# Performance work log

Measured on AMD Instinct MI355X. Metric: run time of the kernel, lower is better.

The kernel has to match this reference:

```python
import jax, jax.numpy as jnp
import numpy as np

B, IN_BITS, NUM_LUTS, K = 1024, 4096, 16384, 6

def setup_inputs() -> dict:
    key = jax.random.key(0)
    k1, k2, k3 = jax.random.split(key, 3)
    x_bits = jax.random.uniform(k1, (B, IN_BITS), dtype=jnp.float32)
    table = jax.random.normal(k2, (NUM_LUTS, 2 ** K), dtype=jnp.float32) * 0.01
    conn_idx = jax.random.randint(k3, (NUM_LUTS, K), 0, IN_BITS, dtype=jnp.int64)
    return {"x_bits": x_bits, "table": table, "conn_idx": conn_idx}

def reference(x_bits, table, conn_idx):
    # threshold to binary bits: [B, IN_BITS]
    bits01 = (x_bits > 0.5)
    # gather connected bits per LUT: [B, NUM_LUTS, K]
    bits = bits01[:, conn_idx]
    # bit-pack (MSB first, matching idx = idx*2 + bit loop): [B, NUM_LUTS]
    powers = (2 ** jnp.arange(K - 1, -1, -1, dtype=jnp.int32))  # [K]
    idx = jnp.sum(bits.astype(jnp.int32) * powers, axis=-1)
    # per-LUT table lookup: table[l, idx[b, l]]
    lut_ids = jnp.arange(NUM_LUTS, dtype=jnp.int32)[None, :]  # [1, NUM_LUTS]
    out = table[lut_ids, idx]  # [B, NUM_LUTS]
    return jax.nn.sigmoid(out)
```

## Files before the change

kernel.cpp:

```cpp
#include <hip/hip_runtime.h>
#include <hip/hip_bf16.h>

constexpr int B        = 1024;
constexpr int IN_BITS  = 4096;
constexpr int NUM_LUTS = 16384;
constexpr int K        = 6;

constexpr int TPB        = 256;
constexpr int LUTS_PER_B = 256;
constexpr int CHUNKS     = 16;
constexpr int BCH        = B / CHUNKS;

constexpr int PACK_BLOCKS = (IN_BITS / TPB) * (B / 32);
constexpr int TBL_BLOCKS  = NUM_LUTS / 64;

__device__ inline unsigned short f2bf(float f) {
    unsigned u = __float_as_uint(f);
    return (unsigned short)((u + 0x7FFFu + ((u >> 16) & 1u)) >> 16);
}

__global__ __launch_bounds__(TPB) void prep_kernel(
    const float* __restrict__ x, const float* __restrict__ table,
    unsigned* __restrict__ packedT, unsigned short* __restrict__ tableT)
{
    __shared__ float tile[64][65];
    const int tid = threadIdx.x;
    const int blk = blockIdx.x;

    if (blk < PACK_BLOCKS) {
        const int pos = (blk % (IN_BITS / TPB)) * TPB + tid;
        const int g   = blk / (IN_BITS / TPB);
        const float* xp = x + (size_t)g * 32 * IN_BITS + pos;
        unsigned word = 0;
#pragma unroll
        for (int j = 0; j < 32; ++j)
            word |= (xp[(size_t)j * IN_BITS] > 0.5f) ? (1u << j) : 0u;
        packedT[(size_t)g * IN_BITS + pos] = word;
    } else {
        const int bt = blk - PACK_BLOCKS;
        const int l0 = bt * 64;
        const float4* src = (const float4*)(table + (size_t)l0 * 64);
#pragma unroll
        for (int i = 0; i < 4; ++i) {
            int q = tid + i * 256;
            float4 v = src[q];
            int l = q >> 4;
            int e = (q & 15) * 4;
            tile[l][e + 0] = v.x; tile[l][e + 1] = v.y;
            tile[l][e + 2] = v.z; tile[l][e + 3] = v.w;
        }
        __syncthreads();
#pragma unroll
        for (int i = 0; i < 4; ++i) {
            int q  = tid + i * 256;
            int e  = q >> 4;
            int lc = (q & 15) * 4;
            ushort4 v;
            v.x = f2bf(1.0f / (1.0f + __expf(-tile[lc + 0][e])));
            v.y = f2bf(1.0f / (1.0f + __expf(-tile[lc + 1][e])));
            v.z = f2bf(1.0f / (1.0f + __expf(-tile[lc + 2][e])));
            v.w = f2bf(1.0f / (1.0f + __expf(-tile[lc + 3][e])));
            ((ushort4*)(tableT + (size_t)e * NUM_LUTS + l0))[q & 15] = v;
        }
    }
}

__global__ __launch_bounds__(TPB, 4) void lut_kernel(
    const int*            __restrict__ conn,
    const unsigned*       __restrict__ packedT,
    const unsigned short* __restrict__ tableT,
    float*                __restrict__ out)
{
    __shared__ unsigned short tbl[64 * LUTS_PER_B];

    const int tid = threadIdx.x;
    const int l0  = blockIdx.x * LUTS_PER_B;
    const int l   = l0 + tid;

    {
        uint4* dst = (uint4*)tbl;
#pragma unroll
        for (int i = 0; i < 8; ++i) {
            int q = tid + i * 256;
            int e = q >> 5;
            int p = q & 31;
            dst[q] = ((const uint4*)(tableT + (size_t)e * NUM_LUTS + l0))[p];
        }
    }

    int c[K];
#pragma unroll
    for (int k = 0; k < K; ++k) c[k] = conn[(size_t)l * K + k];

    __syncthreads();

    const int bbase = blockIdx.y * BCH;
    float* op = out + (size_t)bbase * NUM_LUTS + l;

#pragma unroll
    for (int g = 0; g < BCH / 32; ++g) {
        const unsigned* pr = packedT + (size_t)(bbase / 32 + g) * IN_BITS;
        unsigned w[K];
#pragma unroll
        for (int k = 0; k < K; ++k) w[k] = pr[c[k]];

#pragma unroll
        for (int j = 0; j < 32; ++j) {
            int idx = 0;
#pragma unroll
            for (int k = 0; k < K; ++k)
                idx = (idx << 1) | (int)((w[k] >> j) & 1u);
            unsigned short h = tbl[idx * LUTS_PER_B + tid];
            float v = __uint_as_float((unsigned)h << 16);
            __builtin_nontemporal_store(v, op);
            op += NUM_LUTS;
        }
    }
}

extern "C" void kernel_launch(void* const* d_in, const int* in_sizes, int n_in,
                              void* d_out, int out_size, void* d_ws, size_t ws_size,
                              hipStream_t stream)
{
    const float* x_bits = (const float*)d_in[0];
    const float* table  = (const float*)d_in[1];
    const int*   conn   = (const int*)d_in[2];
    float* out = (float*)d_out;

    unsigned*       packedT = (unsigned*)d_ws;
    unsigned short* tableT  = (unsigned short*)((char*)d_ws + 512 * 1024);

    prep_kernel<<<PACK_BLOCKS + TBL_BLOCKS, TPB, 0, stream>>>(
        x_bits, table, packedT, tableT);

    dim3 g2(NUM_LUTS / LUTS_PER_B, CHUNKS);
    lut_kernel<<<g2, TPB, 0, stream>>>(conn, packedT, tableT, out);
}
```

Before: 93.55 us.

## Fuse prep and LUT kernels into one cooperative kernel with grid sync

Merges the bit-packing/table-transpose prep kernel and the LUT lookup kernel into one cooperatively launched kernel. The grid is 1024 blocks: the first 768 do prep work, then a grid-wide barrier runs before every block does the lookup phase. Both phases share one shared-memory buffer. This removes the second kernel launch and the gap between kernels, but adds a grid barrier and needs all 1024 blocks resident at once. The input x loads also become nontemporal.

```diff
diff --git a/kernel.cpp b/kernel.cpp
--- a/kernel.cpp
+++ b/kernel.cpp
@@ -1,5 +1,8 @@
 #include <hip/hip_runtime.h>
 #include <hip/hip_bf16.h>
+#include <hip/hip_cooperative_groups.h>
+
+namespace cg = cooperative_groups;
 
 constexpr int B        = 1024;
 constexpr int IN_BITS  = 4096;
@@ -13,17 +16,22 @@
 
 constexpr int PACK_BLOCKS = (IN_BITS / TPB) * (B / 32);
 constexpr int TBL_BLOCKS  = NUM_LUTS / 64;
+constexpr int GRID        = (NUM_LUTS / LUTS_PER_B) * CHUNKS;
 
 __device__ inline unsigned short f2bf(float f) {
     unsigned u = __float_as_uint(f);
     return (unsigned short)((u + 0x7FFFu + ((u >> 16) & 1u)) >> 16);
 }
 
-__global__ __launch_bounds__(TPB) void prep_kernel(
-    const float* __restrict__ x, const float* __restrict__ table,
-    unsigned* __restrict__ packedT, unsigned short* __restrict__ tableT)
+__global__ __launch_bounds__(TPB, 4) void fused_kernel(
+    const float*    __restrict__ x,
+    const float*    __restrict__ table,
+    const int*      __restrict__ conn,
+    unsigned*       __restrict__ packedT,
+    unsigned short* __restrict__ tableT,
+    float*          __restrict__ out)
 {
-    __shared__ float tile[64][65];
+    __shared__ char smem[64 * LUTS_PER_B * 2];
     const int tid = threadIdx.x;
     const int blk = blockIdx.x;
 
@@ -33,10 +41,13 @@
         const float* xp = x + (size_t)g * 32 * IN_BITS + pos;
         unsigned word = 0;
 #pragma unroll
-        for (int j = 0; j < 32; ++j)
-            word |= (xp[(size_t)j * IN_BITS] > 0.5f) ? (1u << j) : 0u;
+        for (int j = 0; j < 32; ++j) {
+            float v = __builtin_nontemporal_load(xp + (size_t)j * IN_BITS);
+            word |= (v > 0.5f) ? (1u << j) : 0u;
+        }
         packedT[(size_t)g * IN_BITS + pos] = word;
-    } else {
+    } else if (blk < PACK_BLOCKS + TBL_BLOCKS) {
+        float (*tile)[65] = (float (*)[65])smem;
         const int bt = blk - PACK_BLOCKS;
         const int l0 = bt * 64;
         const float4* src = (const float4*)(table + (size_t)l0 * 64);
@@ -63,19 +74,14 @@
             ((ushort4*)(tableT + (size_t)e * NUM_LUTS + l0))[q & 15] = v;
         }
     }
-}
 
-__global__ __launch_bounds__(TPB, 4) void lut_kernel(
-    const int*            __restrict__ conn,
-    const unsigned*       __restrict__ packedT,
-    const unsigned short* __restrict__ tableT,
-    float*                __restrict__ out)
-{
-    __shared__ unsigned short tbl[64 * LUTS_PER_B];
+    cg::this_grid().sync();
 
-    const int tid = threadIdx.x;
-    const int l0  = blockIdx.x * LUTS_PER_B;
-    const int l   = l0 + tid;
+    unsigned short* tbl = (unsigned short*)smem;
+    const int lutBlk = blk & 63;
+    const int chunk  = blk >> 6;
+    const int l0     = lutBlk * LUTS_PER_B;
+    const int l      = l0 + tid;
 
     {
         uint4* dst = (uint4*)tbl;
@@ -94,7 +100,7 @@
 
     __syncthreads();
 
-    const int bbase = blockIdx.y * BCH;
+    const int bbase = chunk * BCH;
     float* op = out + (size_t)bbase * NUM_LUTS + l;
 
 #pragma unroll
@@ -130,9 +136,8 @@
     unsigned*       packedT = (unsigned*)d_ws;
     unsigned short* tableT  = (unsigned short*)((char*)d_ws + 512 * 1024);
 
-    prep_kernel<<<PACK_BLOCKS + TBL_BLOCKS, TPB, 0, stream>>>(
-        x_bits, table, packedT, tableT);
-
-    dim3 g2(NUM_LUTS / LUTS_PER_B, CHUNKS);
-    lut_kernel<<<g2, TPB, 0, stream>>>(conn, packedT, tableT, out);
+    void* args[] = { (void*)&x_bits, (void*)&table, (void*)&conn,
+                     (void*)&packedT, (void*)&tableT, (void*)&out };
+    hipLaunchCooperativeKernel((void*)fused_kernel, dim3(GRID), dim3(TPB),
+                               args, 0, stream);
 }
```

Measured after the change: 217.6 us. +132.6%, slower.
